# Kernel tuning notes

Measured on AMD Instinct MI355X. Metric: run time of the kernel, lower is better.

The kernel has to match this reference:

```python
import jax, jax.numpy as jnp
import numpy as np


def setup_inputs() -> dict:
    key = jax.random.key(0)
    ks = jax.random.split(key, 4)
    B, H, W, C = 4, 64, 64, 256
    d = C // 8
    x = jax.random.normal(ks[0], (B, H, W, C), dtype=jnp.float32)
    wq = jax.random.normal(ks[1], (C, d), dtype=jnp.float32) * (1.0 / np.sqrt(C))
    wk = jax.random.normal(ks[2], (C, d), dtype=jnp.float32) * (1.0 / np.sqrt(C))
    wv = jax.random.normal(ks[3], (C, C), dtype=jnp.float32) * (1.0 / np.sqrt(C))
    bq = jnp.zeros((d,), dtype=jnp.float32)
    bk = jnp.zeros((d,), dtype=jnp.float32)
    bv = jnp.zeros((C,), dtype=jnp.float32)
    return {"x": x, "wq": wq, "bq": bq, "wk": wk, "bk": bk, "wv": wv, "bv": bv}


def reference(x, wq, bq, wk, bk, wv, bv):
    # x: [B, H, W, C] (channels-last, as in Keras Conv2D default)
    B, H, W, C = x.shape
    N = H * W
    xf = x.reshape(B, N, C)                      # 1x1 conv == per-pixel matmul
    q = xf @ wq + bq                             # [B, N, C//8]
    k = xf @ wk + bk                             # [B, N, C//8]
    v = xf @ wv + bv                             # [B, N, C]
    # NOTE: original module applies NO 1/sqrt(d) scaling.
    attn = jax.nn.softmax(jnp.einsum('bnd,bmd->bnm', q, k), axis=-1)  # [B, N, N]
    out = jnp.einsum('bnm,bmc->bnc', attn, v)    # [B, N, C]
    return out.reshape(B, H, W, C) + x
```

## Files before the change

kernel.cpp:

```cpp
#include <hip/hip_runtime.h>
#include <stdint.h>

typedef _Float16 f16;
typedef f16 half8 __attribute__((ext_vector_type(8)));
typedef f16 half4 __attribute__((ext_vector_type(4)));
typedef float floatx4 __attribute__((ext_vector_type(4)));

#define MFMA_F16(A, B, Cc) __builtin_amdgcn_mfma_f32_16x16x32_f16((A), (B), (Cc), 0, 0, 0)

static constexpr int NB  = 4;
static constexpr int NN  = 4096;
static constexpr int NC  = 256;
static constexpr int ND  = 32;
static constexpr int PIX = NB * NN;
static constexpr int NS  = 4;
static constexpr int KS  = NN / NS;

static constexpr int PADK = 40;
static constexpr int PADP = 72;

__device__ f16 g_WbT[320 * 256];
__device__ f16 g_Qh[(size_t)PIX * ND];
__device__ f16 g_Kh[(size_t)PIX * ND];
__device__ f16 g_VbT[(size_t)NB * NC * NN];
__device__ f16 g_Of[(size_t)NS * PIX * NC];
__device__ float g_m[NS * PIX];
__device__ float g_l[NS * PIX];

__global__ __launch_bounds__(256) void prep_weights(const float* __restrict__ wq,
                                                    const float* __restrict__ wk,
                                                    const float* __restrict__ wv) {
  const int tid = blockIdx.x * 256 + threadIdx.x;
  if (tid >= 320 * 256) return;
  const int j = tid >> 8;
  const int k = tid & 255;
  float v;
  if (j < 32)      v = wq[k * 32 + j];
  else if (j < 64) v = wk[k * 32 + (j - 32)];
  else             v = wv[k * 256 + (j - 64)];
  g_WbT[j * 256 + k] = (f16)v;
}

__global__ __launch_bounds__(256) void proj_qkv(const float* __restrict__ x,
                                                const float* __restrict__ bq,
                                                const float* __restrict__ bk,
                                                const float* __restrict__ bv) {
  __shared__ f16 xs[64 * 32];
  __shared__ f16 wsT[320 * 32];
  __shared__ f16 vt[256 * 64];

  const int tid  = threadIdx.x;
  const int lane = tid & 63;
  const int wid  = tid >> 6;
  const int qd   = lane >> 4;
  const int c16  = lane & 15;
  const int p0   = blockIdx.x * 64;
  const floatx4 zero4 = {0.f, 0.f, 0.f, 0.f};

  floatx4 acc[20];
#pragma unroll
  for (int i = 0; i < 20; ++i) acc[i] = zero4;

  for (int kk = 0; kk < 256; kk += 32) {
    {
      const int r = tid >> 2, g = tid & 3;
      const floatx4* s4 = (const floatx4*)(x + (size_t)(p0 + r) * NC + kk + g * 8);
      const floatx4 xa = s4[0], xb = s4[1];
      half8 h;
      h[0] = (f16)xa[0]; h[1] = (f16)xa[1]; h[2] = (f16)xa[2]; h[3] = (f16)xa[3];
      h[4] = (f16)xb[0]; h[5] = (f16)xb[1]; h[6] = (f16)xb[2]; h[7] = (f16)xb[3];
      *(half8*)&xs[r * 32 + g * 8] = h;
    }
#pragma unroll
    for (int i = 0; i < 10; ++i) {
      const int cid = tid + 256 * i;
      const int j = cid >> 3, m = cid & 7;
      *(half4*)&wsT[j * 32 + m * 4] = *(const half4*)&g_WbT[j * 256 + kk + m * 4];
    }
    __syncthreads();
    const half8 a = *(const half8*)&xs[(wid * 16 + c16) * 32 + qd * 8];
#pragma unroll
    for (int nt = 0; nt < 20; ++nt) {
      const half8 bfr = *(const half8*)&wsT[(nt * 16 + c16) * 32 + qd * 8];
      acc[nt] = MFMA_F16(a, bfr, acc[nt]);
    }
    __syncthreads();
  }

#pragma unroll
  for (int nt = 0; nt < 20; ++nt) {
    const int j = nt * 16 + c16;
    const float bias = (j < 32) ? bq[j] : (j < 64) ? bk[j - 32] : bv[j - 64];
#pragma unroll
    for (int r = 0; r < 4; ++r) {
      const int rl = wid * 16 + qd * 4 + r;
      const int p  = p0 + rl;
      const float val = acc[nt][r] + bias;
      if (j < 32) {
        g_Qh[(size_t)p * ND + j] = (f16)(val * 1.44269504f);
      } else if (j < 64) {
        g_Kh[(size_t)p * ND + (j - 32)] = (f16)val;
      } else {
        vt[(j - 64) * 64 + rl] = (f16)val;
      }
    }
  }
  __syncthreads();
  const int b  = p0 >> 12;
  const int n0 = p0 & (NN - 1);
#pragma unroll
  for (int i = 0; i < 16; ++i) {
    const int cid = tid + 256 * i;
    const int c = cid >> 4, m = cid & 15;
    *(half4*)(g_VbT + ((size_t)(b * NC + c)) * NN + n0 + m * 4) =
        *(const half4*)&vt[c * 64 + m * 4];
  }
}

__global__ __launch_bounds__(256, 2) void attn_split(void) {
  __shared__ f16 ks[64 * PADK];
  __shared__ f16 vsT[2][256 * PADK];
  __shared__ f16 ps[4][2][16 * PADP];

  const int tid  = threadIdx.x;
  const int lane = tid & 63;
  const int wid  = tid >> 6;
  const int qd   = lane >> 4;
  const int c16  = lane & 15;
  const int b    = blockIdx.y;
  const int s    = blockIdx.z;
  const int q0   = blockIdx.x * 128 + wid * 32;
  const floatx4 zero4 = {0.f, 0.f, 0.f, 0.f};

  half8 qf[2];
#pragma unroll
  for (int g = 0; g < 2; ++g)
    qf[g] = *(const half8*)(g_Qh + ((size_t)(b * NN + q0 + g * 16 + c16)) * ND + qd * 8);

  floatx4 acc[2][16];
#pragma unroll
  for (int g = 0; g < 2; ++g)
#pragma unroll
    for (int i = 0; i < 16; ++i) acc[g][i] = zero4;
  float m_i[2] = {-1e30f, -1e30f};
  float l_p[2] = {0.f, 0.f};

  for (int k0 = s * KS; k0 < (s + 1) * KS; k0 += 64) {
    {
      const int row = tid >> 2, part = tid & 3;
      *(half8*)&ks[row * PADK + part * 8] =
          *(const half8*)(g_Kh + ((size_t)(b * NN + k0 + row)) * ND + part * 8);
    }
#pragma unroll
    for (int i = 0; i < 8; ++i) {
      const int id = tid + 256 * i;
      const int c = id >> 3, p = id & 7;
      *(half8*)&vsT[p >> 2][c * PADK + (p & 3) * 8] =
          *(const half8*)(g_VbT + ((size_t)(b * NC + c)) * NN + k0 + p * 8);
    }
    __syncthreads();

    half8 ka[4];
#pragma unroll
    for (int a = 0; a < 4; ++a)
      ka[a] = *(const half8*)&ks[(a * 16 + c16) * PADK + qd * 8];
    floatx4 st[2][4];
#pragma unroll
    for (int g = 0; g < 2; ++g)
#pragma unroll
      for (int a = 0; a < 4; ++a) st[g][a] = MFMA_F16(ka[a], qf[g], zero4);

    float tm[2];
#pragma unroll
    for (int g = 0; g < 2; ++g) {
      float t0 = fmaxf(fmaxf(st[g][0][0], st[g][0][1]), fmaxf(st[g][0][2], st[g][0][3]));
      float t1 = fmaxf(fmaxf(st[g][1][0], st[g][1][1]), fmaxf(st[g][1][2], st[g][1][3]));
      float t2 = fmaxf(fmaxf(st[g][2][0], st[g][2][1]), fmaxf(st[g][2][2], st[g][2][3]));
      float t3 = fmaxf(fmaxf(st[g][3][0], st[g][3][1]), fmaxf(st[g][3][2], st[g][3][3]));
      tm[g] = fmaxf(fmaxf(t0, t1), fmaxf(t2, t3));
    }
    if (__any(tm[0] > m_i[0] || tm[1] > m_i[1])) {
#pragma unroll
      for (int g = 0; g < 2; ++g) {
        float tr = tm[g];
        tr = fmaxf(tr, __shfl_xor(tr, 16));
        tr = fmaxf(tr, __shfl_xor(tr, 32));
        const float m_new = (tr > m_i[g]) ? tr + 5.0f : m_i[g];
        const float alpha = exp2f(m_i[g] - m_new);
        m_i[g] = m_new;
        l_p[g] *= alpha;
        float a4[4];
#pragma unroll
        for (int r = 0; r < 4; ++r) a4[r] = __shfl(alpha, qd * 4 + r);
#pragma unroll
        for (int ct = 0; ct < 16; ++ct)
#pragma unroll
          for (int r = 0; r < 4; ++r) acc[g][ct][r] *= a4[r];
      }
    }

#pragma unroll
    for (int g = 0; g < 2; ++g) {
      float ts = 0.f;
#pragma unroll
      for (int a = 0; a < 4; ++a) {
        half4 h;
#pragma unroll
        for (int r = 0; r < 4; ++r) {
          const float p = exp2f(st[g][a][r] - m_i[g]);
          ts += p;
          h[r] = (f16)p;
        }
        *(half4*)&ps[wid][g][c16 * PADP + a * 16 + qd * 4] = h;
      }
      l_p[g] += ts;
    }
    asm volatile("" ::: "memory");

    half8 pa[2][2];
#pragma unroll
    for (int g = 0; g < 2; ++g)
#pragma unroll
      for (int kh = 0; kh < 2; ++kh)
        pa[g][kh] = *(const half8*)&ps[wid][g][c16 * PADP + kh * 32 + qd * 8];
#pragma unroll
    for (int ct = 0; ct < 16; ++ct) {
#pragma unroll
      for (int kh = 0; kh < 2; ++kh) {
        const half8 bfr = *(const half8*)&vsT[kh][(ct * 16 + c16) * PADK + qd * 8];
        acc[0][ct] = MFMA_F16(pa[0][kh], bfr, acc[0][ct]);
        acc[1][ct] = MFMA_F16(pa[1][kh], bfr, acc[1][ct]);
      }
    }
    __syncthreads();
  }

#pragma unroll
  for (int g = 0; g < 2; ++g) {
    float l = l_p[g];
    l += __shfl_xor(l, 16);
    l += __shfl_xor(l, 32);
    if (qd == 0) {
      const int row = b * NN + q0 + g * 16 + c16;
      g_m[s * PIX + row] = m_i[g];
      g_l[s * PIX + row] = l;
    }
    float linv[4];
#pragma unroll
    for (int r = 0; r < 4; ++r) linv[r] = 1.0f / __shfl(l, qd * 4 + r);
#pragma unroll
    for (int ct = 0; ct < 16; ++ct)
#pragma unroll
      for (int r = 0; r < 4; ++r) {
        const int qrow = q0 + g * 16 + qd * 4 + r;
        const int c = ct * 16 + c16;
        g_Of[((size_t)(s * PIX + b * NN + qrow)) * NC + c] = (f16)(acc[g][ct][r] * linv[r]);
      }
  }
}

__global__ __launch_bounds__(256) void combine(const float* __restrict__ x,
                                               float* __restrict__ out) {
  const int tid  = threadIdx.x;
  const int lane = tid & 63;
  const int wid  = tid >> 6;
  const int row  = blockIdx.x * 4 + wid;
  const int c    = lane * 4;

  float m[NS], l[NS], M = -1e30f;
#pragma unroll
  for (int s = 0; s < NS; ++s) {
    m[s] = g_m[s * PIX + row];
    l[s] = g_l[s * PIX + row];
    M = fmaxf(M, m[s]);
  }
  float w[NS], den = 0.f;
#pragma unroll
  for (int s = 0; s < NS; ++s) { w[s] = l[s] * exp2f(m[s] - M); den += w[s]; }
  const float inv = 1.0f / den;

  float a0 = 0.f, a1 = 0.f, a2 = 0.f, a3 = 0.f;
#pragma unroll
  for (int s = 0; s < NS; ++s) {
    const half4 h = *(const half4*)&g_Of[((size_t)(s * PIX + row)) * NC + c];
    const float ws = w[s] * inv;
    a0 += ws * (float)h[0];
    a1 += ws * (float)h[1];
    a2 += ws * (float)h[2];
    a3 += ws * (float)h[3];
  }
  const floatx4 xv = *(const floatx4*)&x[(size_t)row * NC + c];
  floatx4 o;
  o[0] = a0 + xv[0]; o[1] = a1 + xv[1]; o[2] = a2 + xv[2]; o[3] = a3 + xv[3];
  *(floatx4*)&out[(size_t)row * NC + c] = o;
}

extern "C" void kernel_launch(void* const* d_in, const int* in_sizes, int n_in,
                              void* d_out, int out_size, void* d_ws, size_t ws_size,
                              hipStream_t stream) {
  (void)in_sizes; (void)n_in; (void)d_ws; (void)ws_size; (void)out_size;
  const float* x  = (const float*)d_in[0];
  const float* wq = (const float*)d_in[1];
  const float* bq = (const float*)d_in[2];
  const float* wk = (const float*)d_in[3];
  const float* bk = (const float*)d_in[4];
  const float* wv = (const float*)d_in[5];
  const float* bv = (const float*)d_in[6];
  float* out = (float*)d_out;

  hipLaunchKernelGGL(prep_weights, dim3(320), dim3(256), 0, stream, wq, wk, wv);
  hipLaunchKernelGGL(proj_qkv, dim3(256), dim3(256), 0, stream, x, bq, bk, bv);
  hipLaunchKernelGGL(attn_split, dim3(NN / 128, NB, NS), dim3(256), 0, stream);
  hipLaunchKernelGGL(combine, dim3(PIX / 4), dim3(256), 0, stream, x, out);
}
```

Before: 169.6 us.

## Load V tiles via global_load_lds with XOR swizzle and prefetch K in registers

V tiles now go straight from global memory into LDS with the async global_load_lds path. The LDS layout drops padding for an XOR swizzle, applied both to the V tile and to the P staging buffer. K is no longer staged in LDS but read into registers directly, with the next tile's K prefetched during the PV phase. The aim is to remove register round-trips and padding waste in LDS and to overlap the next tile's loads with compute. In exchange it adds an extra __syncthreads per iteration and relies on implicit waits on the async LDS loads, and it may not actually overlap because the next V load is issued after the barrier.

```diff
diff --git a/kernel.cpp b/kernel.cpp
--- a/kernel.cpp
+++ b/kernel.cpp
@@ -16,9 +16,6 @@
 static constexpr int NS  = 4;
 static constexpr int KS  = NN / NS;
 
-static constexpr int PADK = 40;
-static constexpr int PADP = 72;
-
 __device__ f16 g_WbT[320 * 256];
 __device__ f16 g_Qh[(size_t)PIX * ND];
 __device__ f16 g_Kh[(size_t)PIX * ND];
@@ -26,6 +23,12 @@
 __device__ f16 g_Of[(size_t)NS * PIX * NC];
 __device__ float g_m[NS * PIX];
 __device__ float g_l[NS * PIX];
+
+__device__ inline void gl2lds16(const f16* g, f16* l) {
+  __builtin_amdgcn_global_load_lds(
+      (const __attribute__((address_space(1))) void*)g,
+      (__attribute__((address_space(3))) void*)l, 16, 0, 0);
+}
 
 __global__ __launch_bounds__(256) void prep_weights(const float* __restrict__ wq,
                                                     const float* __restrict__ wk,
@@ -118,9 +121,8 @@
 }
 
 __global__ __launch_bounds__(256, 2) void attn_split(void) {
-  __shared__ f16 ks[64 * PADK];
-  __shared__ f16 vsT[2][256 * PADK];
-  __shared__ f16 ps[4][2][16 * PADP];
+  __shared__ f16 vsT[256 * 64];
+  __shared__ f16 ps[4][2][16 * 64];
 
   const int tid  = threadIdx.x;
   const int lane = tid & 63;
@@ -130,7 +132,13 @@
   const int b    = blockIdx.y;
   const int s    = blockIdx.z;
   const int q0   = blockIdx.x * 128 + wid * 32;
+  const int sx7  = c16 & 7;
   const floatx4 zero4 = {0.f, 0.f, 0.f, 0.f};
+
+  const int vrow = wid * 64 + (lane >> 3);
+  const int vchk = (lane & 7) ^ ((lane >> 3) & 7);
+  const f16* vlane = g_VbT + ((size_t)(b * NC + vrow)) * NN + vchk * 8;
+  f16* vdst = &vsT[(size_t)wid * 4096 + (size_t)0];
 
   half8 qf[2];
 #pragma unroll
@@ -145,30 +153,22 @@
   float m_i[2] = {-1e30f, -1e30f};
   float l_p[2] = {0.f, 0.f};
 
-  for (int k0 = s * KS; k0 < (s + 1) * KS; k0 += 64) {
-    {
-      const int row = tid >> 2, part = tid & 3;
-      *(half8*)&ks[row * PADK + part * 8] =
-          *(const half8*)(g_Kh + ((size_t)(b * NN + k0 + row)) * ND + part * 8);
-    }
-#pragma unroll
-    for (int i = 0; i < 8; ++i) {
-      const int id = tid + 256 * i;
-      const int c = id >> 3, p = id & 7;
-      *(half8*)&vsT[p >> 2][c * PADK + (p & 3) * 8] =
-          *(const half8*)(g_VbT + ((size_t)(b * NC + c)) * NN + k0 + p * 8);
-    }
-    __syncthreads();
-
-    half8 ka[4];
-#pragma unroll
-    for (int a = 0; a < 4; ++a)
-      ka[a] = *(const half8*)&ks[(a * 16 + c16) * PADK + qd * 8];
+  const int kbeg = s * KS, kend = (s + 1) * KS;
+
+#pragma unroll
+  for (int i = 0; i < 8; ++i)
+    gl2lds16(vlane + kbeg + i * 8 * NN, vdst + i * 512);
+  half8 kreg[4];
+#pragma unroll
+  for (int a = 0; a < 4; ++a)
+    kreg[a] = *(const half8*)(g_Kh + ((size_t)(b * NN + kbeg + a * 16 + c16)) * ND + qd * 8);
+
+  for (int k0 = kbeg; k0 < kend; k0 += 64) {
     floatx4 st[2][4];
 #pragma unroll
     for (int g = 0; g < 2; ++g)
 #pragma unroll
-      for (int a = 0; a < 4; ++a) st[g][a] = MFMA_F16(ka[a], qf[g], zero4);
+      for (int a = 0; a < 4; ++a) st[g][a] = MFMA_F16(kreg[a], qf[g], zero4);
 
     float tm[2];
 #pragma unroll
@@ -211,28 +211,45 @@
           ts += p;
           h[r] = (f16)p;
         }
-        *(half4*)&ps[wid][g][c16 * PADP + a * 16 + qd * 4] = h;
+        const int pc = ((a * 2 + (qd >> 1)) ^ sx7) * 8 + (qd & 1) * 4;
+        *(half4*)&ps[wid][g][c16 * 64 + pc] = h;
       }
       l_p[g] += ts;
     }
-    asm volatile("" ::: "memory");
+
+    __syncthreads();
+
+    const int k0n = (k0 + 64 < kend) ? (k0 + 64) : kbeg;
+    half8 knew[4];
+#pragma unroll
+    for (int a = 0; a < 4; ++a)
+      knew[a] = *(const half8*)(g_Kh + ((size_t)(b * NN + k0n + a * 16 + c16)) * ND + qd * 8);
 
     half8 pa[2][2];
 #pragma unroll
     for (int g = 0; g < 2; ++g)
 #pragma unroll
       for (int kh = 0; kh < 2; ++kh)
-        pa[g][kh] = *(const half8*)&ps[wid][g][c16 * PADP + kh * 32 + qd * 8];
+        pa[g][kh] = *(const half8*)&ps[wid][g][c16 * 64 + ((kh * 4 + qd) ^ sx7) * 8];
 #pragma unroll
     for (int ct = 0; ct < 16; ++ct) {
 #pragma unroll
       for (int kh = 0; kh < 2; ++kh) {
-        const half8 bfr = *(const half8*)&vsT[kh][(ct * 16 + c16) * PADK + qd * 8];
+        const half8 bfr =
+            *(const half8*)&vsT[(ct * 16 + c16) * 64 + ((kh * 4 + qd) ^ sx7) * 8];
         acc[0][ct] = MFMA_F16(pa[0][kh], bfr, acc[0][ct]);
         acc[1][ct] = MFMA_F16(pa[1][kh], bfr, acc[1][ct]);
       }
     }
     __syncthreads();
+
+    if (k0 + 64 < kend) {
+#pragma unroll
+      for (int i = 0; i < 8; ++i)
+        gl2lds16(vlane + (k0 + 64) + i * 8 * NN, vdst + i * 512);
+    }
+#pragma unroll
+    for (int a = 0; a < 4; ++a) kreg[a] = knew[a];
   }
 
 #pragma unroll
```

After: 164.9 us. 2.8% less time.
